# Optimization experiments

Measured on AMD Instinct MI355X. Metric: run time of the kernel, lower is better.

Reference implementation:

```python
import math
import jax, jax.numpy as jnp
import numpy as np

B, S, H = 4, 2048, 1024

def setup_inputs() -> dict:
    key = jax.random.key(0)
    k1, k2, k3, k4 = jax.random.split(key, 4)
    X = jax.random.normal(k1, (B, S, H), dtype=jnp.float32)
    attention_mask = jax.random.randint(k2, (B, S), 0, 2).astype(jnp.bool_)
    W = jax.random.normal(k3, (H, 3 * H), dtype=jnp.float32) * (1.0 / math.sqrt(H))
    b = jax.random.normal(k4, (3 * H,), dtype=jnp.float32) * 0.02
    return {"X": X, "attention_mask": attention_mask, "W": W, "b": b}

def reference(X, attention_mask, W, b):
    hidden_dim = X.shape[-1]
    # fused QKV projection: (B,S,3H)
    QKV = X @ W + b
    Q, K, V = jnp.split(QKV, 3, axis=-1)
    # scores: (B, S, S)
    scores = jnp.einsum('bqd,bkd->bqk', Q, K) / math.sqrt(hidden_dim)
    # 2D key-padding mask (B,S) -> broadcast over query dim; True = masked
    mask = attention_mask[:, None, :]  # (B,1,S) broadcasts to (B,S,S)
    scores = jnp.where(mask, -jnp.inf, scores)
    attn = jax.nn.softmax(scores, axis=-1)
    # dropout_rate = 0.0 (eval): identity
    return jnp.einsum('bqk,bkd->bqd', attn, V)
```

## Files before the change

### kernel.cpp

```cpp
#include <hip/hip_runtime.h>
#include <hip/hip_bf16.h>
#include <stdint.h>


typedef __attribute__((ext_vector_type(8))) short bf16x8;
typedef __attribute__((ext_vector_type(4))) float f32x4;

__device__ __forceinline__ void async_cp16(const void* g, void* l) {
  __builtin_amdgcn_global_load_lds(
      (const __attribute__((address_space(1))) void*)g,
      (__attribute__((address_space(3))) void*)l, 16, 0, 0);
}

__global__ void cvt_f32_bf16(const float* __restrict__ s,
                             __hip_bfloat16* __restrict__ d, int n) {
  int i = (blockIdx.x * blockDim.x + threadIdx.x) * 4;
  if (i >= n) return;
  float4 f = *(const float4*)(s + i);
  __hip_bfloat16 o[4];
  o[0] = __float2bfloat16(f.x);
  o[1] = __float2bfloat16(f.y);
  o[2] = __float2bfloat16(f.z);
  o[3] = __float2bfloat16(f.w);
  *(ushort4*)(d + i) = *(const ushort4*)o;
}

__global__ void transpose_cvt_f32(const float* __restrict__ src, int srcld,
                                  __hip_bfloat16* __restrict__ dst, int dstld) {
  __shared__ float tile[32][33];
  int bx = blockIdx.x * 32;
  int by = blockIdx.y * 32;
  int tx = threadIdx.x, ty = threadIdx.y;
#pragma unroll
  for (int j = 0; j < 4; ++j)
    tile[ty + j * 8][tx] = src[(int64_t)(by + ty + j * 8) * srcld + bx + tx];
  __syncthreads();
#pragma unroll
  for (int j = 0; j < 4; ++j)
    dst[(int64_t)(bx + ty + j * 8) * dstld + by + tx] =
        __float2bfloat16(tile[tx][ty + j * 8]);
}

__global__ __launch_bounds__(256) void mask_scan(const int* __restrict__ mask,
                                                 int* __restrict__ idx,
                                                 int* __restrict__ cnt,
                                                 int* __restrict__ cnt_pad) {
  const int b = blockIdx.x;
  mask += b * 2048;
  idx += b * 2048;
  const int t = threadIdx.x;
  const int lane = t & 63, wave = t >> 6;

  int keep[8];
  int local = 0;
#pragma unroll
  for (int j = 0; j < 8; ++j) {
    keep[j] = (mask[t * 8 + j] == 0);
    local += keep[j];
  }
  int pre = local;
#pragma unroll
  for (int off = 1; off <= 32; off <<= 1) {
    int n = __shfl_up(pre, off, 64);
    if (lane >= off) pre += n;
  }
  __shared__ int wsum[4];
  if (lane == 63) wsum[wave] = pre;
  __syncthreads();
  int base = 0;
  for (int w = 0; w < wave; ++w) base += wsum[w];
  int excl = base + pre - local;
#pragma unroll
  for (int j = 0; j < 8; ++j)
    if (keep[j]) idx[excl++] = t * 8 + j;
  if (t == 255) {
    int tot = base + pre;
    cnt[b] = tot;
    cnt_pad[b] = (tot + 127) & ~127;
  }
}

__global__ __launch_bounds__(256) void gemm_qkv(
    const __hip_bfloat16* __restrict__ Xb, const __hip_bfloat16* __restrict__ Wt,
    const float* __restrict__ bias, const int* __restrict__ idx,
    const int* __restrict__ cnt, const int* __restrict__ cnt_pad,
    __hip_bfloat16* __restrict__ Q, __hip_bfloat16* __restrict__ Kc,
    __hip_bfloat16* __restrict__ Vt) {
  const int z = blockIdx.z;
  const int f = blockIdx.x;
  const int xcd = f & 7, loc = f >> 3;
  const int m0 = ((loc & 7) * 2 + (xcd >> 2)) * 128;
  const int n_idx = (loc >> 3) * 4 + (xcd & 3);
  const bool isQ = (n_idx < 8);
  if (!isQ && m0 >= cnt_pad[z]) return;
  const int n0 = (isQ ? n_idx : n_idx - 8) * 128;
  const __hip_bfloat16* A = Xb + (int64_t)z * 2048 * 1024;
  const __hip_bfloat16* Bt = Wt + (isQ ? 0 : (int64_t)1024 * 1024);
  const float* bv = bias + (isQ ? 0 : 1024);

  const int tid = threadIdx.x;
  const int wave = tid >> 6, lane = tid & 63;
  const int quad = lane >> 4, tr = lane & 15;
  const int wm = wave & 1, wn = wave >> 1;

  __shared__ __hip_bfloat16 ls[17408];
  __hip_bfloat16* lsA = ls;
  __hip_bfloat16* lsB = ls + 8192;

  const __hip_bfloat16* gsrc[8];
  __hip_bfloat16* ldst[8];
  {
    const int srow = lane >> 3;
    const int kc = (((lane & 7) ^ srow) * 8);
    const int cz = isQ ? 0 : cnt[z];
    const int* idxz = idx + z * 2048;
#pragma unroll
    for (int cc = 0; cc < 8; ++cc) {
      int c = wave * 8 + cc;
      int isA = (c < 16);
      int cr = isA ? c : (c - 16);
      int row = cr * 8 + srow;
      if (isA) {
        int ar = m0 + row;
        if (!isQ) ar = (ar < cz) ? idxz[ar] : 0;
        gsrc[cc] = A + (int64_t)ar * 1024 + kc;
      } else {
        gsrc[cc] = Bt + (int64_t)(n0 + row) * 1024 + kc;
      }
      ldst[cc] = (isA ? lsA : lsB) + cr * 512;
    }
  }

  f32x4 acc[4][4];
#pragma unroll
  for (int mi = 0; mi < 4; ++mi)
#pragma unroll
    for (int ni = 0; ni < 4; ++ni) acc[mi][ni] = (f32x4){0.f, 0.f, 0.f, 0.f};

  const int t7 = tr & 7;

  for (int k0 = 0; k0 < 1024; k0 += 64) {
    __syncthreads();
#pragma unroll
    for (int cc = 0; cc < 8; ++cc) async_cp16(gsrc[cc] + k0, ldst[cc]);
    __syncthreads();

#pragma unroll
    for (int w = 0; w < 2; ++w) {
      const int sl = ((w << 2) | quad) ^ t7;
      bf16x8 af[4], bfv[4];
#pragma unroll
      for (int mi = 0; mi < 4; ++mi)
        af[mi] = *(const bf16x8*)(lsA + (wm * 64 + mi * 16 + tr) * 64 + sl * 8);
#pragma unroll
      for (int ni = 0; ni < 4; ++ni)
        bfv[ni] = *(const bf16x8*)(lsB + (wn * 64 + ni * 16 + tr) * 64 + sl * 8);
#pragma unroll
      for (int mi = 0; mi < 4; ++mi)
#pragma unroll
        for (int ni = 0; ni < 4; ++ni)
          acc[mi][ni] = __builtin_amdgcn_mfma_f32_16x16x32_bf16(
              af[mi], bfv[ni], acc[mi][ni], 0, 0, 0);
    }
  }

  const int rowbase = m0 + wm * 64;
  const int colbase = n0 + wn * 64;
  if (isQ) {
    __hip_bfloat16* C = Q + (int64_t)z * 2048 * 1024;
#pragma unroll
    for (int ni = 0; ni < 4; ++ni) {
      int col = colbase + ni * 16 + tr;
      float bb = bv[col];
#pragma unroll
      for (int mi = 0; mi < 4; ++mi) {
        int row = rowbase + mi * 16 + quad * 4;
#pragma unroll
        for (int r = 0; r < 4; ++r)
          C[(int64_t)(row + r) * 1024 + col] =
              __float2bfloat16(acc[mi][ni][r] + bb);
      }
    }
  } else if (n0 < 1024) {
    __hip_bfloat16* C = Kc + (int64_t)z * 2048 * 1024;
#pragma unroll
    for (int ni = 0; ni < 4; ++ni) {
      int col = colbase + ni * 16 + tr;
      float bb = bv[col];
#pragma unroll
      for (int mi = 0; mi < 4; ++mi) {
        int row = rowbase + mi * 16 + quad * 4;
#pragma unroll
        for (int r = 0; r < 4; ++r)
          C[(int64_t)(row + r) * 1024 + col] =
              __float2bfloat16(acc[mi][ni][r] + bb);
      }
    }
  } else {
    __syncthreads();
#pragma unroll
    for (int ni = 0; ni < 4; ++ni) {
      int cl = wn * 64 + ni * 16 + tr;
      float bb = bv[colbase + ni * 16 + tr];
#pragma unroll
      for (int mi = 0; mi < 4; ++mi) {
        int rl = wm * 64 + mi * 16 + quad * 4;
        __hip_bfloat16 h[4];
#pragma unroll
        for (int r = 0; r < 4; ++r) h[r] = __float2bfloat16(acc[mi][ni][r] + bb);
        *(ushort4*)(ls + cl * 136 + rl) = *(const ushort4*)h;
      }
    }
    __syncthreads();
    __hip_bfloat16* Vz = Vt + (int64_t)z * 1024 * 2048;
    const int d0 = n0 - 1024;
    const int seg = tid & 15;
#pragma unroll
    for (int p = 0; p < 8; ++p) {
      int d = p * 16 + (tid >> 4);
      bf16x8 v = *(const bf16x8*)(ls + d * 136 + seg * 8);
      *(bf16x8*)(Vz + (int64_t)(d0 + d) * 2048 + m0 + seg * 8) = v;
    }
  }
}

__global__ __launch_bounds__(256) void gemm_scores(
    const __hip_bfloat16* __restrict__ Qb, const __hip_bfloat16* __restrict__ Kc,
    __hip_bfloat16* __restrict__ Sc, float* __restrict__ rowsum,
    const int* __restrict__ cnt, const int* __restrict__ cnt_pad,
    float scale2) {
  const int z = blockIdx.z;
  const int f = blockIdx.x;
  const int xcd = f & 7, loc = f >> 3;
  const int m0 = ((loc & 7) * 2 + (xcd >> 2)) * 128;
  const int n0 = ((loc >> 3) * 4 + (xcd & 3)) * 64;
  if (n0 >= cnt_pad[z]) return;
  const __hip_bfloat16* A = Qb + (int64_t)z * 2048 * 1024;
  const __hip_bfloat16* Bt = Kc + (int64_t)z * 2048 * 1024;

  const int tid = threadIdx.x;
  const int wave = tid >> 6, lane = tid & 63;
  const int quad = lane >> 4, tr = lane & 15;
  const int wm = wave & 1, wn = wave >> 1;

  __shared__ __hip_bfloat16 lsA[128 * 64];
  __shared__ __hip_bfloat16 lsB[64 * 64];

  const __hip_bfloat16* gsrc[6];
  __hip_bfloat16* ldst[6];
  {
    const int srow = lane >> 3;
    const int kc = (((lane & 7) ^ srow) * 8);
#pragma unroll
    for (int cc = 0; cc < 6; ++cc) {
      int c = wave * 6 + cc;
      int isA = (c < 16);
      int cr = isA ? c : (c - 16);
      int row = cr * 8 + srow;
      gsrc[cc] = isA ? (A + (int64_t)(m0 + row) * 1024 + kc)
                     : (Bt + (int64_t)(n0 + row) * 1024 + kc);
      ldst[cc] = (isA ? lsA : lsB) + cr * 512;
    }
  }

  f32x4 acc[4][2];
#pragma unroll
  for (int mi = 0; mi < 4; ++mi)
#pragma unroll
    for (int ni = 0; ni < 2; ++ni) acc[mi][ni] = (f32x4){0.f, 0.f, 0.f, 0.f};

  const int t7 = tr & 7;

  for (int k0 = 0; k0 < 1024; k0 += 64) {
    __syncthreads();
#pragma unroll
    for (int cc = 0; cc < 6; ++cc) async_cp16(gsrc[cc] + k0, ldst[cc]);
    __syncthreads();

#pragma unroll
    for (int w = 0; w < 2; ++w) {
      const int sl = ((w << 2) | quad) ^ t7;
      bf16x8 af[4], bfv[2];
#pragma unroll
      for (int mi = 0; mi < 4; ++mi)
        af[mi] = *(const bf16x8*)(lsA + (wm * 64 + mi * 16 + tr) * 64 + sl * 8);
#pragma unroll
      for (int ni = 0; ni < 2; ++ni)
        bfv[ni] = *(const bf16x8*)(lsB + (wn * 32 + ni * 16 + tr) * 64 + sl * 8);
#pragma unroll
      for (int mi = 0; mi < 4; ++mi)
#pragma unroll
        for (int ni = 0; ni < 2; ++ni)
          acc[mi][ni] = __builtin_amdgcn_mfma_f32_16x16x32_bf16(
              af[mi], bfv[ni], acc[mi][ni], 0, 0, 0);
    }
  }

  const int rowbase = m0 + wm * 64;
  const int colbase = n0 + wn * 32;
  const int cn = cnt[z];
  __hip_bfloat16* C = Sc + (int64_t)z * 2048 * 2048;

  float psum[4][4];
#pragma unroll
  for (int mi = 0; mi < 4; ++mi)
#pragma unroll
    for (int r = 0; r < 4; ++r) psum[mi][r] = 0.f;

#pragma unroll
  for (int ni = 0; ni < 2; ++ni) {
    int col = colbase + ni * 16 + tr;
    bool valid = (col < cn);
#pragma unroll
    for (int mi = 0; mi < 4; ++mi) {
      int row = rowbase + mi * 16 + quad * 4;
#pragma unroll
      for (int r = 0; r < 4; ++r) {
        float e = valid ? exp2f(acc[mi][ni][r] * scale2) : 0.f;
        C[(int64_t)(row + r) * 2048 + col] = __float2bfloat16(e);
        psum[mi][r] += e;
      }
    }
  }
#pragma unroll
  for (int off = 1; off <= 8; off <<= 1)
#pragma unroll
    for (int mi = 0; mi < 4; ++mi)
#pragma unroll
      for (int r = 0; r < 4; ++r)
        psum[mi][r] += __shfl_xor(psum[mi][r], off, 64);
  if (tr == 0) {
    float* rs = rowsum + z * 2048 + rowbase;
#pragma unroll
    for (int mi = 0; mi < 4; ++mi)
#pragma unroll
      for (int r = 0; r < 4; ++r)
        atomicAdd(&rs[mi * 16 + quad * 4 + r], psum[mi][r]);
  }
}

__global__ __launch_bounds__(256) void gemm_pv(
    const __hip_bfloat16* __restrict__ Sc, const __hip_bfloat16* __restrict__ Vt,
    float* __restrict__ out, const float* __restrict__ rowsum,
    const int* __restrict__ cnt_pad) {
  const int z = blockIdx.z;
  const int f = blockIdx.x;
  const int xcd = f & 7, loc = f >> 3;
  const int m0 = ((loc & 7) * 2 + (xcd >> 2)) * 128;
  const int n0 = ((loc >> 3) * 4 + (xcd & 3)) * 64;
  const int Ks = cnt_pad[z];
  const __hip_bfloat16* A = Sc + (int64_t)z * 2048 * 2048;
  const __hip_bfloat16* Bt = Vt + (int64_t)z * 1024 * 2048;

  const int tid = threadIdx.x;
  const int wave = tid >> 6, lane = tid & 63;
  const int quad = lane >> 4, tr = lane & 15;
  const int wm = wave & 1, wn = wave >> 1;

  __shared__ __hip_bfloat16 lsA[128 * 64];
  __shared__ __hip_bfloat16 lsB[64 * 64];

  const __hip_bfloat16* gsrc[6];
  __hip_bfloat16* ldst[6];
  {
    const int srow = lane >> 3;
    const int kc = (((lane & 7) ^ srow) * 8);
#pragma unroll
    for (int cc = 0; cc < 6; ++cc) {
      int c = wave * 6 + cc;
      int isA = (c < 16);
      int cr = isA ? c : (c - 16);
      int row = cr * 8 + srow;
      gsrc[cc] = isA ? (A + (int64_t)(m0 + row) * 2048 + kc)
                     : (Bt + (int64_t)(n0 + row) * 2048 + kc);
      ldst[cc] = (isA ? lsA : lsB) + cr * 512;
    }
  }

  f32x4 acc[4][2];
#pragma unroll
  for (int mi = 0; mi < 4; ++mi)
#pragma unroll
    for (int ni = 0; ni < 2; ++ni) acc[mi][ni] = (f32x4){0.f, 0.f, 0.f, 0.f};

  const int t7 = tr & 7;

  for (int k0 = 0; k0 < Ks; k0 += 64) {
    __syncthreads();
#pragma unroll
    for (int cc = 0; cc < 6; ++cc) async_cp16(gsrc[cc] + k0, ldst[cc]);
    __syncthreads();

#pragma unroll
    for (int w = 0; w < 2; ++w) {
      const int sl = ((w << 2) | quad) ^ t7;
      bf16x8 af[4], bfv[2];
#pragma unroll
      for (int mi = 0; mi < 4; ++mi)
        af[mi] = *(const bf16x8*)(lsA + (wm * 64 + mi * 16 + tr) * 64 + sl * 8);
#pragma unroll
      for (int ni = 0; ni < 2; ++ni)
        bfv[ni] = *(const bf16x8*)(lsB + (wn * 32 + ni * 16 + tr) * 64 + sl * 8);
#pragma unroll
      for (int mi = 0; mi < 4; ++mi)
#pragma unroll
        for (int ni = 0; ni < 2; ++ni)
          acc[mi][ni] = __builtin_amdgcn_mfma_f32_16x16x32_bf16(
              af[mi], bfv[ni], acc[mi][ni], 0, 0, 0);
    }
  }

  const int rowbase = m0 + wm * 64;
  const int colbase = n0 + wn * 32;
  const float* rs = rowsum + z * 2048 + rowbase;
  float invv[4][4];
#pragma unroll
  for (int mi = 0; mi < 4; ++mi)
#pragma unroll
    for (int r = 0; r < 4; ++r) invv[mi][r] = 1.0f / rs[mi * 16 + quad * 4 + r];

  float* C = out + (int64_t)z * 2048 * 1024;
#pragma unroll
  for (int ni = 0; ni < 2; ++ni) {
    int col = colbase + ni * 16 + tr;
#pragma unroll
    for (int mi = 0; mi < 4; ++mi) {
      int row = rowbase + mi * 16 + quad * 4;
#pragma unroll
      for (int r = 0; r < 4; ++r)
        C[(int64_t)(row + r) * 1024 + col] = acc[mi][ni][r] * invv[mi][r];
    }
  }
}

extern "C" void kernel_launch(void* const* d_in, const int* in_sizes, int n_in,
                              void* d_out, int out_size, void* d_ws,
                              size_t ws_size, hipStream_t stream) {
  const float* X = (const float*)d_in[0];
  const int* mask = (const int*)d_in[1];
  const float* W = (const float*)d_in[2];
  const float* bias = (const float*)d_in[3];
  float* out = (float*)d_out;

  char* ws = (char*)d_ws;
  auto alloc = [&](size_t bytes) {
    char* p = ws;
    ws += (bytes + 255) & ~(size_t)255;
    return p;
  };
  __hip_bfloat16* Xb = (__hip_bfloat16*)alloc(8192ULL * 1024 * 2);
  __hip_bfloat16* Wt = (__hip_bfloat16*)alloc(3072ULL * 1024 * 2);
  __hip_bfloat16* Q = (__hip_bfloat16*)alloc(8192ULL * 1024 * 2);
  __hip_bfloat16* Kc = (__hip_bfloat16*)alloc(4ULL * 2048 * 1024 * 2);
  __hip_bfloat16* Vt = (__hip_bfloat16*)alloc(4ULL * 1024 * 2048 * 2);
  __hip_bfloat16* Sc = (__hip_bfloat16*)alloc(4ULL * 2048 * 2048 * 2);
  float* rowsum = (float*)alloc(8192ULL * 4);
  int* idx = (int*)alloc(4ULL * 2048 * 4);
  int* cnt = (int*)alloc(64);
  int* cnt_pad = (int*)alloc(64);

  hipMemsetAsync(rowsum, 0, 8192ULL * 4, stream);
  cvt_f32_bf16<<<8192, 256, 0, stream>>>(X, Xb, 8192 * 1024);
  transpose_cvt_f32<<<dim3(96, 32, 1), dim3(32, 8), 0, stream>>>(W, 3072, Wt,
                                                                 1024);
  mask_scan<<<4, 256, 0, stream>>>(mask, idx, cnt, cnt_pad);
  gemm_qkv<<<dim3(384, 1, 4), 256, 0, stream>>>(Xb, Wt, bias, idx, cnt,
                                                cnt_pad, Q, Kc, Vt);
  gemm_scores<<<dim3(512, 1, 4), 256, 0, stream>>>(
      Q, Kc, Sc, rowsum, cnt, cnt_pad, 0.03125f * 1.4426950408889634f);
  gemm_pv<<<dim3(256, 1, 4), 256, 0, stream>>>(Sc, Vt, out, rowsum, cnt_pad);
}
```

Baseline: 222.7 us.

## Double-buffer LDS loads and enlarge score/PV tiles to 128x128

All three GEMM kernels now use a two-stage LDS ping-pong: the next K-slice is fetched with async global-to-LDS copies while the current one is consumed by MFMAs, with explicit vmcnt waits and barriers. LDS fragment reads use inline ds_read_b128 with precomputed base addresses and immediate offsets. The scores and PV kernels grow from 128x64 to 128x128 tiles, which halves their grid sizes and improves operand reuse. The cost is more LDS per block (64KB), lower occupancy, and the PV loop now steps K in 128-wide pairs.

Result: faster. 204.7 us (-8.1%).

```diff
diff --git a/kernel.cpp b/kernel.cpp
--- a/kernel.cpp
+++ b/kernel.cpp
@@ -11,6 +11,26 @@
       (const __attribute__((address_space(1))) void*)g,
       (__attribute__((address_space(3))) void*)l, 16, 0, 0);
 }
+
+__device__ __forceinline__ uint32_t laddr(const void* p) {
+  return (uint32_t)(uintptr_t)(const __attribute__((address_space(3))) void*)p;
+}
+
+#define FENCE() asm volatile("" ::: "memory")
+#define BAR()                           \
+  do {                                  \
+    FENCE();                            \
+    __builtin_amdgcn_s_barrier();       \
+    FENCE();                            \
+  } while (0)
+#define VMW(N) asm volatile("s_waitcnt vmcnt(" #N ")" ::: "memory")
+#define LGKM0()                                            \
+  do {                                                     \
+    asm volatile("s_waitcnt lgkmcnt(0)" ::: "memory");     \
+    __builtin_amdgcn_sched_barrier(0);                     \
+  } while (0)
+#define DSR(dst, a, OFF) \
+  asm volatile("ds_read_b128 %0, %1 offset:" #OFF : "=v"(dst) : "v"(a))
 
 __global__ void cvt_f32_bf16(const float* __restrict__ s,
                              __hip_bfloat16* __restrict__ d, int n) {
@@ -100,18 +120,16 @@
 
   const int tid = threadIdx.x;
   const int wave = tid >> 6, lane = tid & 63;
-  const int quad = lane >> 4, tr = lane & 15;
+  const int quad = lane >> 4, tr = lane & 15, t7 = tr & 7;
   const int wm = wave & 1, wn = wave >> 1;
 
-  __shared__ __hip_bfloat16 ls[17408];
-  __hip_bfloat16* lsA = ls;
-  __hip_bfloat16* lsB = ls + 8192;
+  __shared__ __hip_bfloat16 ls[32768];
 
   const __hip_bfloat16* gsrc[8];
-  __hip_bfloat16* ldst[8];
+  int loff[8];
   {
     const int srow = lane >> 3;
-    const int kc = (((lane & 7) ^ srow) * 8);
+    const int kcs = (((lane & 7) ^ srow) * 8);
     const int cz = isQ ? 0 : cnt[z];
     const int* idxz = idx + z * 2048;
 #pragma unroll
@@ -123,12 +141,25 @@
       if (isA) {
         int ar = m0 + row;
         if (!isQ) ar = (ar < cz) ? idxz[ar] : 0;
-        gsrc[cc] = A + (int64_t)ar * 1024 + kc;
+        gsrc[cc] = A + (int64_t)ar * 1024 + kcs;
       } else {
-        gsrc[cc] = Bt + (int64_t)(n0 + row) * 1024 + kc;
-      }
-      ldst[cc] = (isA ? lsA : lsB) + cr * 512;
-    }
+        gsrc[cc] = Bt + (int64_t)(n0 + row) * 1024 + kcs;
+      }
+      loff[cc] = (isA ? 0 : 8192) + cr * 512;
+    }
+  }
+
+  uint32_t aAd[2][2], bBd[2][2];
+  {
+    uint32_t base = laddr(ls);
+#pragma unroll
+    for (int b = 0; b < 2; ++b)
+#pragma unroll
+      for (int w = 0; w < 2; ++w) {
+        uint32_t col = (uint32_t)(((((w << 2) | quad)) ^ t7) * 16);
+        aAd[b][w] = base + b * 32768 + (wm * 64 + tr) * 128 + col;
+        bBd[b][w] = base + b * 32768 + 16384 + (wn * 64 + tr) * 128 + col;
+      }
   }
 
   f32x4 acc[4][4];
@@ -137,32 +168,50 @@
 #pragma unroll
     for (int ni = 0; ni < 4; ++ni) acc[mi][ni] = (f32x4){0.f, 0.f, 0.f, 0.f};
 
-  const int t7 = tr & 7;
-
-  for (int k0 = 0; k0 < 1024; k0 += 64) {
-    __syncthreads();
-#pragma unroll
-    for (int cc = 0; cc < 8; ++cc) async_cp16(gsrc[cc] + k0, ldst[cc]);
-    __syncthreads();
-
-#pragma unroll
-    for (int w = 0; w < 2; ++w) {
-      const int sl = ((w << 2) | quad) ^ t7;
-      bf16x8 af[4], bfv[4];
-#pragma unroll
-      for (int mi = 0; mi < 4; ++mi)
-        af[mi] = *(const bf16x8*)(lsA + (wm * 64 + mi * 16 + tr) * 64 + sl * 8);
-#pragma unroll
-      for (int ni = 0; ni < 4; ++ni)
-        bfv[ni] = *(const bf16x8*)(lsB + (wn * 64 + ni * 16 + tr) * 64 + sl * 8);
-#pragma unroll
-      for (int mi = 0; mi < 4; ++mi)
-#pragma unroll
-        for (int ni = 0; ni < 4; ++ni)
-          acc[mi][ni] = __builtin_amdgcn_mfma_f32_16x16x32_bf16(
-              af[mi], bfv[ni], acc[mi][ni], 0, 0, 0);
-    }
-  }
+  bf16x8 af[4], bf[4];
+
+#define STAGE(BUF, k0)                                            \
+  do {                                                            \
+    _Pragma("unroll") for (int cc = 0; cc < 8; ++cc)              \
+        async_cp16(gsrc[cc] + (k0), ls + (BUF)*16384 + loff[cc]); \
+  } while (0)
+#define COMP(BUF)                                                             \
+  do {                                                                        \
+    _Pragma("unroll") for (int w = 0; w < 2; ++w) {                           \
+      DSR(af[0], aAd[BUF][w], 0);                                             \
+      DSR(af[1], aAd[BUF][w], 2048);                                          \
+      DSR(af[2], aAd[BUF][w], 4096);                                          \
+      DSR(af[3], aAd[BUF][w], 6144);                                          \
+      DSR(bf[0], bBd[BUF][w], 0);                                             \
+      DSR(bf[1], bBd[BUF][w], 2048);                                          \
+      DSR(bf[2], bBd[BUF][w], 4096);                                          \
+      DSR(bf[3], bBd[BUF][w], 6144);                                          \
+      LGKM0();                                                                \
+      _Pragma("unroll") for (int mi = 0; mi < 4; ++mi)                        \
+          _Pragma("unroll") for (int ni = 0; ni < 4; ++ni) acc[mi][ni] =      \
+              __builtin_amdgcn_mfma_f32_16x16x32_bf16(af[mi], bf[ni],         \
+                                                      acc[mi][ni], 0, 0, 0);  \
+    }                                                                         \
+  } while (0)
+
+  STAGE(0, 0);
+  for (int it = 0; it < 8; ++it) {
+    STAGE(1, (2 * it + 1) * 64);
+    VMW(8); BAR();
+    COMP(0);
+    BAR();
+    if (it < 7) {
+      STAGE(0, (2 * it + 2) * 64);
+      VMW(8);
+    } else {
+      VMW(0);
+    }
+    BAR();
+    COMP(1);
+    BAR();
+  }
+#undef STAGE
+#undef COMP
 
   const int rowbase = m0 + wm * 64;
   const int colbase = n0 + wn * 64;
@@ -233,71 +282,101 @@
   const int f = blockIdx.x;
   const int xcd = f & 7, loc = f >> 3;
   const int m0 = ((loc & 7) * 2 + (xcd >> 2)) * 128;
-  const int n0 = ((loc >> 3) * 4 + (xcd & 3)) * 64;
+  const int n0 = ((loc >> 3) * 4 + (xcd & 3)) * 128;
   if (n0 >= cnt_pad[z]) return;
   const __hip_bfloat16* A = Qb + (int64_t)z * 2048 * 1024;
   const __hip_bfloat16* Bt = Kc + (int64_t)z * 2048 * 1024;
 
   const int tid = threadIdx.x;
   const int wave = tid >> 6, lane = tid & 63;
-  const int quad = lane >> 4, tr = lane & 15;
+  const int quad = lane >> 4, tr = lane & 15, t7 = tr & 7;
   const int wm = wave & 1, wn = wave >> 1;
 
-  __shared__ __hip_bfloat16 lsA[128 * 64];
-  __shared__ __hip_bfloat16 lsB[64 * 64];
-
-  const __hip_bfloat16* gsrc[6];
-  __hip_bfloat16* ldst[6];
+  __shared__ __hip_bfloat16 ls[32768];
+
+  const __hip_bfloat16* gsrc[8];
+  int loff[8];
   {
     const int srow = lane >> 3;
-    const int kc = (((lane & 7) ^ srow) * 8);
-#pragma unroll
-    for (int cc = 0; cc < 6; ++cc) {
-      int c = wave * 6 + cc;
+    const int kcs = (((lane & 7) ^ srow) * 8);
+#pragma unroll
+    for (int cc = 0; cc < 8; ++cc) {
+      int c = wave * 8 + cc;
       int isA = (c < 16);
       int cr = isA ? c : (c - 16);
       int row = cr * 8 + srow;
-      gsrc[cc] = isA ? (A + (int64_t)(m0 + row) * 1024 + kc)
-                     : (Bt + (int64_t)(n0 + row) * 1024 + kc);
-      ldst[cc] = (isA ? lsA : lsB) + cr * 512;
-    }
-  }
-
-  f32x4 acc[4][2];
+      gsrc[cc] = isA ? (A + (int64_t)(m0 + row) * 1024 + kcs)
+                     : (Bt + (int64_t)(n0 + row) * 1024 + kcs);
+      loff[cc] = (isA ? 0 : 8192) + cr * 512;
+    }
+  }
+
+  uint32_t aAd[2][2], bBd[2][2];
+  {
+    uint32_t base = laddr(ls);
+#pragma unroll
+    for (int b = 0; b < 2; ++b)
+#pragma unroll
+      for (int w = 0; w < 2; ++w) {
+        uint32_t col = (uint32_t)(((((w << 2) | quad)) ^ t7) * 16);
+        aAd[b][w] = base + b * 32768 + (wm * 64 + tr) * 128 + col;
+        bBd[b][w] = base + b * 32768 + 16384 + (wn * 64 + tr) * 128 + col;
+      }
+  }
+
+  f32x4 acc[4][4];
 #pragma unroll
   for (int mi = 0; mi < 4; ++mi)
 #pragma unroll
-    for (int ni = 0; ni < 2; ++ni) acc[mi][ni] = (f32x4){0.f, 0.f, 0.f, 0.f};
-
-  const int t7 = tr & 7;
-
-  for (int k0 = 0; k0 < 1024; k0 += 64) {
-    __syncthreads();
-#pragma unroll
-    for (int cc = 0; cc < 6; ++cc) async_cp16(gsrc[cc] + k0, ldst[cc]);
-    __syncthreads();
-
-#pragma unroll
-    for (int w = 0; w < 2; ++w) {
-      const int sl = ((w << 2) | quad) ^ t7;
-      bf16x8 af[4], bfv[2];
-#pragma unroll
-      for (int mi = 0; mi < 4; ++mi)
-        af[mi] = *(const bf16x8*)(lsA + (wm * 64 + mi * 16 + tr) * 64 + sl * 8);
-#pragma unroll
-      for (int ni = 0; ni < 2; ++ni)
-        bfv[ni] = *(const bf16x8*)(lsB + (wn * 32 + ni * 16 + tr) * 64 + sl * 8);
-#pragma unroll
-      for (int mi = 0; mi < 4; ++mi)
-#pragma unroll
-        for (int ni = 0; ni < 2; ++ni)
-          acc[mi][ni] = __builtin_amdgcn_mfma_f32_16x16x32_bf16(
-              af[mi], bfv[ni], acc[mi][ni], 0, 0, 0);
-    }
-  }
+    for (int ni = 0; ni < 4; ++ni) acc[mi][ni] = (f32x4){0.f, 0.f, 0.f, 0.f};
+
+  bf16x8 af[4], bf[4];
+
+#define STAGE(BUF, k0)                                            \
+  do {                                                            \
+    _Pragma("unroll") for (int cc = 0; cc < 8; ++cc)              \
+        async_cp16(gsrc[cc] + (k0), ls + (BUF)*16384 + loff[cc]); \
+  } while (0)
+#define COMP(BUF)                                                             \
+  do {                                                                        \
+    _Pragma("unroll") for (int w = 0; w < 2; ++w) {                           \
+      DSR(af[0], aAd[BUF][w], 0);                                             \
+      DSR(af[1], aAd[BUF][w], 2048);                                          \
+      DSR(af[2], aAd[BUF][w], 4096);                                          \
+      DSR(af[3], aAd[BUF][w], 6144);                                          \
+      DSR(bf[0], bBd[BUF][w], 0);                                             \
+      DSR(bf[1], bBd[BUF][w], 2048);                                          \
+      DSR(bf[2], bBd[BUF][w], 4096);                                          \
+      DSR(bf[3], bBd[BUF][w], 6144);                                          \
+      LGKM0();                                                                \
+      _Pragma("unroll") for (int mi = 0; mi < 4; ++mi)                        \
+          _Pragma("unroll") for (int ni = 0; ni < 4; ++ni) acc[mi][ni] =      \
+              __builtin_amdgcn_mfma_f32_16x16x32_bf16(af[mi], bf[ni],         \
+                                                      acc[mi][ni], 0, 0, 0);  \
+    }                                                                         \
+  } while (0)
+
+  STAGE(0, 0);
+  for (int it = 0; it < 8; ++it) {
+    STAGE(1, (2 * it + 1) * 64);
+    VMW(8); BAR();
+    COMP(0);
+    BAR();
+    if (it < 7) {
+      STAGE(0, (2 * it + 2) * 64);
+      VMW(8);
+    } else {
+      VMW(0);
+    }
+    BAR();
+    COMP(1);
+    BAR();
+  }
+#undef STAGE
+#undef COMP
 
   const int rowbase = m0 + wm * 64;
-  const int colbase = n0 + wn * 32;
+  const int colbase = n0 + wn * 64;
   const int cn = cnt[z];
   __hip_bfloat16* C = Sc + (int64_t)z * 2048 * 2048;
 
@@ -308,7 +387,7 @@
     for (int r = 0; r < 4; ++r) psum[mi][r] = 0.f;
 
 #pragma unroll
-  for (int ni = 0; ni < 2; ++ni) {
+  for (int ni = 0; ni < 4; ++ni) {
     int col = colbase + ni * 16 + tr;
     bool valid = (col < cn);
 #pragma unroll
@@ -347,71 +426,102 @@
   const int f = blockIdx.x;
   const int xcd = f & 7, loc = f >> 3;
   const int m0 = ((loc & 7) * 2 + (xcd >> 2)) * 128;
-  const int n0 = ((loc >> 3) * 4 + (xcd & 3)) * 64;
+  const int n0 = ((loc >> 3) * 4 + (xcd & 3)) * 128;
   const int Ks = cnt_pad[z];
   const __hip_bfloat16* A = Sc + (int64_t)z * 2048 * 2048;
   const __hip_bfloat16* Bt = Vt + (int64_t)z * 1024 * 2048;
 
   const int tid = threadIdx.x;
   const int wave = tid >> 6, lane = tid & 63;
-  const int quad = lane >> 4, tr = lane & 15;
+  const int quad = lane >> 4, tr = lane & 15, t7 = tr & 7;
   const int wm = wave & 1, wn = wave >> 1;
 
-  __shared__ __hip_bfloat16 lsA[128 * 64];
-  __shared__ __hip_bfloat16 lsB[64 * 64];
-
-  const __hip_bfloat16* gsrc[6];
-  __hip_bfloat16* ldst[6];
+  __shared__ __hip_bfloat16 ls[32768];
+
+  const __hip_bfloat16* gsrc[8];
+  int loff[8];
   {
     const int srow = lane >> 3;
-    const int kc = (((lane & 7) ^ srow) * 8);
-#pragma unroll
-    for (int cc = 0; cc < 6; ++cc) {
-      int c = wave * 6 + cc;
+    const int kcs = (((lane & 7) ^ srow) * 8);
+#pragma unroll
+    for (int cc = 0; cc < 8; ++cc) {
+      int c = wave * 8 + cc;
       int isA = (c < 16);
       int cr = isA ? c : (c - 16);
       int row = cr * 8 + srow;
-      gsrc[cc] = isA ? (A + (int64_t)(m0 + row) * 2048 + kc)
-                     : (Bt + (int64_t)(n0 + row) * 2048 + kc);
-      ldst[cc] = (isA ? lsA : lsB) + cr * 512;
-    }
-  }
-
-  f32x4 acc[4][2];
+      gsrc[cc] = isA ? (A + (int64_t)(m0 + row) * 2048 + kcs)
+                     : (Bt + (int64_t)(n0 + row) * 2048 + kcs);
+      loff[cc] = (isA ? 0 : 8192) + cr * 512;
+    }
+  }
+
+  uint32_t aAd[2][2], bBd[2][2];
+  {
+    uint32_t base = laddr(ls);
+#pragma unroll
+    for (int b = 0; b < 2; ++b)
+#pragma unroll
+      for (int w = 0; w < 2; ++w) {
+        uint32_t col = (uint32_t)(((((w << 2) | quad)) ^ t7) * 16);
+        aAd[b][w] = base + b * 32768 + (wm * 64 + tr) * 128 + col;
+        bBd[b][w] = base + b * 32768 + 16384 + (wn * 64 + tr) * 128 + col;
+      }
+  }
+
+  f32x4 acc[4][4];
 #pragma unroll
   for (int mi = 0; mi < 4; ++mi)
 #pragma unroll
-    for (int ni = 0; ni < 2; ++ni) acc[mi][ni] = (f32x4){0.f, 0.f, 0.f, 0.f};
-
-  const int t7 = tr & 7;
-
-  for (int k0 = 0; k0 < Ks; k0 += 64) {
-    __syncthreads();
-#pragma unroll
-    for (int cc = 0; cc < 6; ++cc) async_cp16(gsrc[cc] + k0, ldst[cc]);
-    __syncthreads();
-
-#pragma unroll
-    for (int w = 0; w < 2; ++w) {
-      const int sl = ((w << 2) | quad) ^ t7;
-      bf16x8 af[4], bfv[2];
-#pragma unroll
-      for (int mi = 0; mi < 4; ++mi)
-        af[mi] = *(const bf16x8*)(lsA + (wm * 64 + mi * 16 + tr) * 64 + sl * 8);
-#pragma unroll
-      for (int ni = 0; ni < 2; ++ni)
-        bfv[ni] = *(const bf16x8*)(lsB + (wn * 32 + ni * 16 + tr) * 64 + sl * 8);
-#pragma unroll
-      for (int mi = 0; mi < 4; ++mi)
-#pragma unroll
-        for (int ni = 0; ni < 2; ++ni)
-          acc[mi][ni] = __builtin_amdgcn_mfma_f32_16x16x32_bf16(
-              af[mi], bfv[ni], acc[mi][ni], 0, 0, 0);
-    }
-  }
+    for (int ni = 0; ni < 4; ++ni) acc[mi][ni] = (f32x4){0.f, 0.f, 0.f, 0.f};
+
+  bf16x8 af[4], bf[4];
+
+#define STAGE(BUF, k0)                                            \
+  do {                                                            \
+    _Pragma("unroll") for (int cc = 0; cc < 8; ++cc)              \
+        async_cp16(gsrc[cc] + (k0), ls + (BUF)*16384 + loff[cc]); \
+  } while (0)
+#define COMP(BUF)                                                             \
+  do {                                                                        \
+    _Pragma("unroll") for (int w = 0; w < 2; ++w) {                           \
+      DSR(af[0], aAd[BUF][w], 0);                                             \
+      DSR(af[1], aAd[BUF][w], 2048);                                          \
+      DSR(af[2], aAd[BUF][w], 4096);                                          \
+      DSR(af[3], aAd[BUF][w], 6144);                                          \
+      DSR(bf[0], bBd[BUF][w], 0);                                             \
+      DSR(bf[1], bBd[BUF][w], 2048);                                          \
+      DSR(bf[2], bBd[BUF][w], 4096);                                          \
+      DSR(bf[3], bBd[BUF][w], 6144);                                          \
+      LGKM0();                                                                \
+      _Pragma("unroll") for (int mi = 0; mi < 4; ++mi)                        \
+          _Pragma("unroll") for (int ni = 0; ni < 4; ++ni) acc[mi][ni] =      \
+              __builtin_amdgcn_mfma_f32_16x16x32_bf16(af[mi], bf[ni],         \
+                                                      acc[mi][ni], 0, 0, 0);  \
+    }                                                                         \
+  } while (0)
+
+  const int NP = Ks >> 7;
+  STAGE(0, 0);
+  for (int it = 0; it < NP; ++it) {
+    STAGE(1, (2 * it + 1) * 64);
+    VMW(8); BAR();
+    COMP(0);
+    BAR();
+    if (it + 1 < NP) {
+      STAGE(0, (2 * it + 2) * 64);
+      VMW(8);
+    } else {
+      VMW(0);
+    }
+    BAR();
+    COMP(1);
+    BAR();
+  }
+#undef STAGE
+#undef COMP
 
   const int rowbase = m0 + wm * 64;
-  const int colbase = n0 + wn * 32;
+  const int colbase = n0 + wn * 64;
   const float* rs = rowsum + z * 2048 + rowbase;
   float invv[4][4];
 #pragma unroll
@@ -421,7 +531,7 @@
 
   float* C = out + (int64_t)z * 2048 * 1024;
 #pragma unroll
-  for (int ni = 0; ni < 2; ++ni) {
+  for (int ni = 0; ni < 4; ++ni) {
     int col = colbase + ni * 16 + tr;
 #pragma unroll
     for (int mi = 0; mi < 4; ++mi) {
@@ -466,7 +576,7 @@
   mask_scan<<<4, 256, 0, stream>>>(mask, idx, cnt, cnt_pad);
   gemm_qkv<<<dim3(384, 1, 4), 256, 0, stream>>>(Xb, Wt, bias, idx, cnt,
                                                 cnt_pad, Q, Kc, Vt);
-  gemm_scores<<<dim3(512, 1, 4), 256, 0, stream>>>(
+  gemm_scores<<<dim3(256, 1, 4), 256, 0, stream>>>(
       Q, Kc, Sc, rowsum, cnt, cnt_pad, 0.03125f * 1.4426950408889634f);
-  gemm_pv<<<dim3(256, 1, 4), 256, 0, stream>>>(Sc, Vt, out, rowsum, cnt_pad);
-}
+  gemm_pv<<<dim3(128, 1, 4), 256, 0, stream>>>(Sc, Vt, out, rowsum, cnt_pad);
+}
```
